# Optimization experiments

Measured on AMD Instinct MI355X. Metric: run time of the kernel, lower is better.

Reference implementation:

```python
import jax, jax.numpy as jnp
import numpy as np
import math

H = 16        # num heads
D = 64        # head dim
HID = 1024    # hidden size
MULT = 2      # GIN MLP multiplier
FRAC = 0.1    # top_k fraction of available predecessors
THR = 0.2     # threshold value
BASE = 10000.0  # rope base
CHUNK = 32    # query-row chunk for max aggregator
NEG = -1e30


def _rope(x, pos):
    # x: (b, H, S, D); pos: (b, S) int
    d = x.shape[-1]
    inv = 1.0 / (BASE ** (jnp.arange(0, d, 2, dtype=jnp.float32) / d))
    ang = pos.astype(jnp.float32)[..., None] * inv            # (b, S, d//2)
    cos = jnp.concatenate([jnp.cos(ang)] * 2, -1)[:, None]    # (b, 1, S, d)
    sin = jnp.concatenate([jnp.sin(ang)] * 2, -1)[:, None]
    x1, x2 = jnp.split(x, 2, axis=-1)
    return x * cos + jnp.concatenate([-x2, x1], -1) * sin


def _scaled_topk_causal(adj):
    # faithful vectorization of scaled_topk_causal_4d: per query row i, keep
    # top max(1, ceil(FRAC*i)) of the (threshold-filtered) strict predecessors.
    S = adj.shape[-1]
    j = jnp.arange(S)
    strict = j[None, :] < j[:, None]                           # (S, S) j < i
    # torch: filtered = a[:, :i] * (a >= thr)  -> below-threshold become 0
    filtered = jnp.where(strict, jnp.where(adj >= THR, adj, 0.0), NEG)
    order = jnp.argsort(-filtered, axis=-1)                    # descending, stable
    rank = jnp.argsort(order, axis=-1)                         # inverse permutation
    k = jnp.maximum(1, jnp.ceil(FRAC * jnp.arange(S, dtype=jnp.float32))).astype(jnp.int32)
    k = k.at[0].set(0)                                         # row 0 has no predecessors
    return ((rank < k[None, None, :, None]) & strict).astype(adj.dtype)


def reference(hidden_states, Wq, Wk, Wv, Wo, W1, W2, eps, position_ids):
    b, S, _ = hidden_states.shape
    q = (hidden_states @ Wq).reshape(b, S, H, D).transpose(0, 2, 1, 3)
    kk = (hidden_states @ Wk).reshape(b, S, H, D).transpose(0, 2, 1, 3)
    v = (hidden_states @ Wv).reshape(b, S, H, D).transpose(0, 2, 1, 3)
    q = _rope(q, position_ids)
    kk = _rope(kk, position_ids)
    scores = jnp.einsum('bhid,bhjd->bhij', q, kk) / math.sqrt(D)
    adj = _scaled_topk_causal(scores)                          # binary (b,H,S,S)
    deg = adj.sum(-1)                                          # (b,H,S)
    denom = jnp.maximum(deg, 1.0)[..., None]
    s_agg = jnp.einsum('bhij,bhjd->bhid', adj, v)              # sum
    m_agg = s_agg / denom                                      # mean
    var = jnp.maximum(jnp.einsum('bhij,bhjd->bhid', adj, v * v) / denom - m_agg ** 2, 0.0)
    # max aggregator: masked max over selected predecessors, chunked over rows
    nc = S // CHUNK
    adj_c = jnp.moveaxis(adj.reshape(b, H, nc, CHUNK, S), 2, 0)  # (nc,b,H,C,S)
    mx = jax.lax.map(
        lambda ac: jnp.max(jnp.where(ac[..., None] > 0, v[:, :, None, :, :], NEG), axis=-2),
        adj_c)                                                 # (nc,b,H,C,D)
    mx = jnp.moveaxis(mx, 0, 2).reshape(b, H, S, D)
    mx = jnp.where(deg[..., None] > 0, mx, 0.0)
    comb = jnp.concatenate([s_agg, m_agg, mx, var], -1)        # (b,H,S,4D)
    h1 = jax.nn.silu(jnp.einsum('bhsf,hfm->bhsm', comb, W1))   # per-head GIN MLP
    head_out = jnp.einsum('bhsm,hmd->bhsd', h1, W2) + eps * v  # epsilon-scaled residual
    return head_out.transpose(0, 2, 1, 3).reshape(b, S, H * D) @ Wo


def setup_inputs() -> dict:
    key = jax.random.key(0)
    ks = jax.random.split(key, 8)
    b, S = 1, 1024
    sc = 0.02
    return {
        'hidden_states': jax.random.normal(ks[0], (b, S, HID), jnp.float32),
        'Wq': jax.random.normal(ks[1], (HID, H * D), jnp.float32) * sc,
        'Wk': jax.random.normal(ks[2], (HID, H * D), jnp.float32) * sc,
        'Wv': jax.random.normal(ks[3], (HID, H * D), jnp.float32) * sc,
        'Wo': jax.random.normal(ks[4], (H * D, HID), jnp.float32) * sc,
        'W1': jax.random.normal(ks[5], (H, 4 * D, MULT * D), jnp.float32) * sc,
        'W2': jax.random.normal(ks[6], (H, MULT * D, D), jnp.float32) * sc,
        'eps': jnp.asarray(0.1, jnp.float32),
        'position_ids': jnp.arange(S, dtype=jnp.int32)[None, :],
    }
```

## Files before the change

kernel.cpp:

```cpp
#include <hip/hip_runtime.h>
#include <math.h>

#define NEGF  -1e30f
#define TAU   1e-6f

static __device__ __forceinline__ int imin(int a, int b) { return a < b ? a : b; }

template <int MODE>
__global__ __launch_bounds__(256) void gemm64(
    const float* __restrict__ A, const float* __restrict__ B, float* __restrict__ C,
    const float* __restrict__ R, const float* __restrict__ eps_p,
    int M, int N, int K, int lda, int ldb, int ldc,
    long sA, long sB, long sC)
{
  const int z = blockIdx.z;
  A += (long)z * sA;
  B += (long)z * sB;
  float* Cf = C + (long)z * sC;
  const float* Rz = (MODE == 2) ? (R + (long)z * sC) : nullptr;

  const int bm = blockIdx.x * 64;
  const int bn = blockIdx.y * 64;
  const int tid = threadIdx.x;
  const int r0 = (tid >> 4) * 4;
  const int c0 = (tid & 15) * 4;

  __shared__ float As[16][68];
  __shared__ float Bs[16][64];

  float acc[4][4] = {};

  const int ar = tid >> 2;
  const int ac = (tid & 3) * 4;
  const int br = tid >> 4;
  const int bc = (tid & 15) * 4;

  for (int kt = 0; kt < K; kt += 16) {
    float4 av = *(const float4*)(A + (long)(bm + ar) * lda + kt + ac);
    float4 bv = *(const float4*)(B + (long)(kt + br) * ldb + bn + bc);
    As[ac + 0][ar] = av.x;
    As[ac + 1][ar] = av.y;
    As[ac + 2][ar] = av.z;
    As[ac + 3][ar] = av.w;
    *(float4*)&Bs[br][bc] = bv;
    __syncthreads();
#pragma unroll
    for (int kk = 0; kk < 16; ++kk) {
      const float4 xa = *(const float4*)&As[kk][r0];
      const float4 yb = *(const float4*)&Bs[kk][c0];
      acc[0][0] += xa.x * yb.x; acc[0][1] += xa.x * yb.y; acc[0][2] += xa.x * yb.z; acc[0][3] += xa.x * yb.w;
      acc[1][0] += xa.y * yb.x; acc[1][1] += xa.y * yb.y; acc[1][2] += xa.y * yb.z; acc[1][3] += xa.y * yb.w;
      acc[2][0] += xa.z * yb.x; acc[2][1] += xa.z * yb.y; acc[2][2] += xa.z * yb.z; acc[2][3] += xa.z * yb.w;
      acc[3][0] += xa.w * yb.x; acc[3][1] += xa.w * yb.y; acc[3][2] += xa.w * yb.z; acc[3][3] += xa.w * yb.w;
    }
    __syncthreads();
  }

  const float ev = (MODE == 2) ? eps_p[0] : 0.0f;
#pragma unroll
  for (int e = 0; e < 4; ++e)
#pragma unroll
    for (int f = 0; f < 4; ++f) {
      const int r = bm + r0 + e;
      const int c = bn + c0 + f;
      float x = acc[e][f];
      if (MODE == 1) x = x / (1.0f + expf(-x));
      if (MODE == 2) x += ev * Rz[(long)r * ldc + c];
      Cf[(long)r * ldc + c] = x;
    }
}

__global__ __launch_bounds__(256) void gemm_qkv(
    const float* __restrict__ A,
    const float* __restrict__ Wq, const float* __restrict__ Wk, const float* __restrict__ Wv,
    float* __restrict__ qo, float* __restrict__ ko, float* __restrict__ vo)
{
  const int z = blockIdx.z;
  const float* B = (z == 0) ? Wq : (z == 1) ? Wk : Wv;
  float* C = (z == 0) ? qo : (z == 1) ? ko : vo;

  const int bm = blockIdx.x * 64;
  const int bn = blockIdx.y * 64;
  const int tid = threadIdx.x;
  const int r0 = (tid >> 4) * 4;
  const int c0 = (tid & 15) * 4;

  __shared__ float As[2][32][68];
  __shared__ float Bs[2][32][64];

  float acc[4][4] = {};
  float tot[4][4] = {};

  const int ar = tid >> 2;
  const int ac = (tid & 3) * 8;
  const int br = tid >> 3;
  const int bc = (tid & 7) * 8;

  {
    float4 a0 = *(const float4*)(A + (long)(bm + ar) * 1024 + ac);
    float4 a1 = *(const float4*)(A + (long)(bm + ar) * 1024 + ac + 4);
    float4 b0 = *(const float4*)(B + (long)br * 1024 + bn + bc);
    float4 b1 = *(const float4*)(B + (long)br * 1024 + bn + bc + 4);
    As[0][ac + 0][ar] = a0.x; As[0][ac + 1][ar] = a0.y;
    As[0][ac + 2][ar] = a0.z; As[0][ac + 3][ar] = a0.w;
    As[0][ac + 4][ar] = a1.x; As[0][ac + 5][ar] = a1.y;
    As[0][ac + 6][ar] = a1.z; As[0][ac + 7][ar] = a1.w;
    *(float4*)&Bs[0][br][bc] = b0;
    *(float4*)&Bs[0][br][bc + 4] = b1;
  }
  __syncthreads();

  int cur = 0;
  for (int kt = 0; kt < 1024; kt += 32) {
    const bool more = (kt + 32 < 1024);
    float4 a0n, a1n, b0n, b1n;
    if (more) {
      a0n = *(const float4*)(A + (long)(bm + ar) * 1024 + kt + 32 + ac);
      a1n = *(const float4*)(A + (long)(bm + ar) * 1024 + kt + 32 + ac + 4);
      b0n = *(const float4*)(B + (long)(kt + 32 + br) * 1024 + bn + bc);
      b1n = *(const float4*)(B + (long)(kt + 32 + br) * 1024 + bn + bc + 4);
    }
    if (kt == 384 || kt == 768) {
#pragma unroll
      for (int e = 0; e < 4; ++e)
#pragma unroll
        for (int f = 0; f < 4; ++f) {
          tot[e][f] = __fadd_rn(tot[e][f], acc[e][f]);
          acc[e][f] = 0.0f;
        }
    }
#pragma unroll
    for (int kk = 0; kk < 32; ++kk) {
      const float4 xa = *(const float4*)&As[cur][kk][r0];
      const float4 yb = *(const float4*)&Bs[cur][kk][c0];
      acc[0][0] += xa.x * yb.x; acc[0][1] += xa.x * yb.y; acc[0][2] += xa.x * yb.z; acc[0][3] += xa.x * yb.w;
      acc[1][0] += xa.y * yb.x; acc[1][1] += xa.y * yb.y; acc[1][2] += xa.y * yb.z; acc[1][3] += xa.y * yb.w;
      acc[2][0] += xa.z * yb.x; acc[2][1] += xa.z * yb.y; acc[2][2] += xa.z * yb.z; acc[2][3] += xa.z * yb.w;
      acc[3][0] += xa.w * yb.x; acc[3][1] += xa.w * yb.y; acc[3][2] += xa.w * yb.z; acc[3][3] += xa.w * yb.w;
    }
    if (more) {
      const int nxt = cur ^ 1;
      As[nxt][ac + 0][ar] = a0n.x; As[nxt][ac + 1][ar] = a0n.y;
      As[nxt][ac + 2][ar] = a0n.z; As[nxt][ac + 3][ar] = a0n.w;
      As[nxt][ac + 4][ar] = a1n.x; As[nxt][ac + 5][ar] = a1n.y;
      As[nxt][ac + 6][ar] = a1n.z; As[nxt][ac + 7][ar] = a1n.w;
      *(float4*)&Bs[nxt][br][bc] = b0n;
      *(float4*)&Bs[nxt][br][bc + 4] = b1n;
      __syncthreads();
      cur = nxt;
    }
  }

#pragma unroll
  for (int e = 0; e < 4; ++e)
#pragma unroll
    for (int f = 0; f < 4; ++f)
      C[(long)(bm + r0 + e) * 1024 + bn + c0 + f] = __fadd_rn(tot[e][f], acc[e][f]);
}

__global__ __launch_bounds__(256) void gemm_out(
    const float* __restrict__ A, const float* __restrict__ B, float* __restrict__ C)
{
  const int bm = blockIdx.x * 32;
  const int bn = blockIdx.y * 64;
  const int tid = threadIdx.x;
  const int r0 = (tid >> 4) * 2;
  const int c0 = (tid & 15) * 4;

  __shared__ float As[2][16][36];
  __shared__ float Bs[2][16][64];

  float acc[2][4] = {};

  const int ar = tid >> 3;
  const int ac = (tid & 7) * 2;
  const int br = tid >> 4;
  const int bc = (tid & 15) * 4;

  {
    float2 av = *(const float2*)(A + (long)(bm + ar) * 1024 + ac);
    float4 bv = *(const float4*)(B + (long)br * 1024 + bn + bc);
    As[0][ac + 0][ar] = av.x;
    As[0][ac + 1][ar] = av.y;
    *(float4*)&Bs[0][br][bc] = bv;
  }
  __syncthreads();

  int cur = 0;
  for (int kt = 0; kt < 1024; kt += 16) {
    const bool more = (kt + 16 < 1024);
    float2 avn;
    float4 bvn;
    if (more) {
      avn = *(const float2*)(A + (long)(bm + ar) * 1024 + kt + 16 + ac);
      bvn = *(const float4*)(B + (long)(kt + 16 + br) * 1024 + bn + bc);
    }
#pragma unroll
    for (int kk = 0; kk < 16; ++kk) {
      const float2 xa = *(const float2*)&As[cur][kk][r0];
      const float4 yb = *(const float4*)&Bs[cur][kk][c0];
      acc[0][0] += xa.x * yb.x; acc[0][1] += xa.x * yb.y; acc[0][2] += xa.x * yb.z; acc[0][3] += xa.x * yb.w;
      acc[1][0] += xa.y * yb.x; acc[1][1] += xa.y * yb.y; acc[1][2] += xa.y * yb.z; acc[1][3] += xa.y * yb.w;
    }
    if (more) {
      const int nxt = cur ^ 1;
      As[nxt][ac + 0][ar] = avn.x;
      As[nxt][ac + 1][ar] = avn.y;
      *(float4*)&Bs[nxt][br][bc] = bvn;
      __syncthreads();
      cur = nxt;
    }
  }

#pragma unroll
  for (int e = 0; e < 2; ++e)
#pragma unroll
    for (int f = 0; f < 4; ++f)
      C[(long)(bm + r0 + e) * 1024 + bn + c0 + f] = acc[e][f];
}

__global__ __launch_bounds__(256) void rope_kernel(float* __restrict__ q,
                                                   float* __restrict__ kb,
                                                   const int* __restrict__ pos_ids)
{
  const int g = blockIdx.x * blockDim.x + threadIdx.x;
  const int t = g & 31;
  const int h = (g >> 5) & 15;
  const int s = (g >> 9) & 1023;
  const int buf = g >> 19;
  float* p = buf ? kb : q;

  const float e = (float)(2 * t) / 64.0f;
  const float p32 = (float)pow(10000.0, (double)e);
  const float inv = __fdiv_rn(1.0f, p32);
  const float posf = (float)pos_ids[s];
  const float ang = __fmul_rn(posf, inv);
  const float c  = (float)cos((double)ang);
  const float sn = (float)sin((double)ang);

  const int base = s * 1024 + h * 64;
  const float x1 = p[base + t];
  const float x2 = p[base + t + 32];
  p[base + t]      = __fadd_rn(__fmul_rn(x1, c), __fmul_rn(-x2, sn));
  p[base + t + 32] = __fadd_rn(__fmul_rn(x2, c), __fmul_rn(x1, sn));
}

__global__ __launch_bounds__(256) void gemm_score(
    const float* __restrict__ q, const float* __restrict__ kb,
    float* __restrict__ S, int headBase)
{
  const int x = blockIdx.x;
  int bmT = 0;
  while ((bmT + 1) * (bmT + 2) / 2 <= x) ++bmT;
  const int bnT = x - bmT * (bmT + 1) / 2;

  const int hl = blockIdx.y;
  const int off = (headBase + hl) * 64;
  const int bm = bmT * 64;
  const int bn = bnT * 64;
  const int tid = threadIdx.x;
  const int r0 = (tid >> 4) * 4;
  const int c0 = (tid & 15) * 4;

  __shared__ float As[16][68];
  __shared__ float Bs[16][68];

  float acc[4][4] = {};

  const int ar = tid >> 2;
  const int ac = (tid & 3) * 4;

  for (int kt = 0; kt < 64; kt += 16) {
    float4 av = *(const float4*)(q  + (long)(bm + ar) * 1024 + off + kt + ac);
    float4 bv = *(const float4*)(kb + (long)(bn + ar) * 1024 + off + kt + ac);
    As[ac + 0][ar] = av.x; As[ac + 1][ar] = av.y;
    As[ac + 2][ar] = av.z; As[ac + 3][ar] = av.w;
    Bs[ac + 0][ar] = bv.x; Bs[ac + 1][ar] = bv.y;
    Bs[ac + 2][ar] = bv.z; Bs[ac + 3][ar] = bv.w;
    __syncthreads();
#pragma unroll
    for (int kk = 0; kk < 16; ++kk) {
      const float4 xa = *(const float4*)&As[kk][r0];
      const float4 yb = *(const float4*)&Bs[kk][c0];
      acc[0][0] += xa.x * yb.x; acc[0][1] += xa.x * yb.y; acc[0][2] += xa.x * yb.z; acc[0][3] += xa.x * yb.w;
      acc[1][0] += xa.y * yb.x; acc[1][1] += xa.y * yb.y; acc[1][2] += xa.y * yb.z; acc[1][3] += xa.y * yb.w;
      acc[2][0] += xa.z * yb.x; acc[2][1] += xa.z * yb.y; acc[2][2] += xa.z * yb.z; acc[2][3] += xa.z * yb.w;
      acc[3][0] += xa.w * yb.x; acc[3][1] += xa.w * yb.y; acc[3][2] += xa.w * yb.z; acc[3][3] += xa.w * yb.w;
    }
    __syncthreads();
  }

#pragma unroll
  for (int e = 0; e < 4; ++e)
#pragma unroll
    for (int f = 0; f < 4; ++f)
      S[((long)hl * 1024 + bm + r0 + e) * 1024 + bn + c0 + f] = acc[e][f] * 0.125f;
}

__global__ __launch_bounds__(256) void select_agg2(
    const float* __restrict__ S, const float* __restrict__ v,
    float* __restrict__ comb, int headBase)
{
  const int i = blockIdx.x;
  const int hl = blockIdx.y;
  const int h = headBase + hl;
  const int tid = threadIdx.x;
  const int lane = tid & 63;
  const int wid = tid >> 6;

  __shared__ int hist[256];
  __shared__ int wtot[4];
  __shared__ int selBinSh, newRkSh, selCntSh;
  __shared__ unsigned vminSh;
  __shared__ int mInIdx;
  __shared__ unsigned WBits;
  __shared__ int outIdxMin;
  __shared__ unsigned long long tbIn, tbOut;
  __shared__ int hypOut, hypIn;
  __shared__ int listLen;
  __shared__ unsigned list[128];
  __shared__ float red[6][4][64];

  if (tid == 0) {
    mInIdx = -1; WBits = 0u; outIdxMin = 0x7FFFFFFF;
    tbIn = ~0ull; tbOut = ~0ull; hypOut = -1; hypIn = -1; listLen = 0;
  }

  const int cs = (i + 255) >> 8;
  const int j0 = tid * cs;
  const int j1 = imin(j0 + cs, i);
  const int nj = (j1 > j0) ? (j1 - j0) : 0;

  float rawr[4];
  unsigned uf[4];
  const float* row = S + ((long)hl * 1024 + i) * 1024;
  for (int m = 0; m < nj; ++m) {
    const float rv = row[j0 + m];
    rawr[m] = rv;
    uf[m] = __float_as_uint((rv >= 0.2f) ? rv : 0.0f);
  }

  const int kk = (i > 0) ? (i + 9) / 10 : 0;
  unsigned V = 0u;
  int need_eq = 0;
  unsigned char f0[4] = {0, 0, 0, 0};

  if (kk > 0) {
    unsigned prefix = 0;
    int rk = kk;
    bool done = false;
    for (int pass = 0; pass < 4; ++pass) {
      const int shift = 24 - 8 * pass;
      hist[tid] = 0;
      __syncthreads();
      for (int m = 0; m < nj; ++m) {
        const unsigned u = uf[m];
        const bool active = (pass == 0) || ((u >> (shift + 8)) == prefix);
        if (active) atomicAdd(&hist[(u >> shift) & 0xFF], 1);
      }
      __syncthreads();
      const int hval = hist[tid];
      int val = hval;
#pragma unroll
      for (int off = 1; off < 64; off <<= 1) {
        int n = __shfl_up(val, off, 64);
        if (lane >= off) val += n;
      }
      if (lane == 63) wtot[wid] = val;
      __syncthreads();
      int wpre = 0;
      for (int w = 0; w < wid; ++w) wpre += wtot[w];
      const int incl = wpre + val;
      const int total = wtot[0] + wtot[1] + wtot[2] + wtot[3];
      const int sfx = total - incl + hval;
      if (sfx >= rk && (sfx - hval) < rk) {
        selBinSh = tid;
        newRkSh = rk - (sfx - hval);
        selCntSh = hval;
      }
      __syncthreads();
      const int selBin = selBinSh;
      prefix = (prefix << 8) | (unsigned)selBin;
      rk = newRkSh;
      const int scnt = selCntSh;
      if (pass == 0 && selBin == 0) {
        V = 0u; need_eq = rk; done = true;
      } else if (rk == scnt) {
        if (tid == 0) vminSh = 0xFFFFFFFFu;
        __syncthreads();
        for (int m = 0; m < nj; ++m)
          if (uf[m] != 0u && (uf[m] >> shift) == prefix) atomicMin(&vminSh, uf[m]);
        __syncthreads();
        V = vminSh; need_eq = 0x3FFFFFFF; done = true;
      }
      if (done) break;
    }
    if (!done) { V = prefix; need_eq = rk; }

    int e = 0;
    for (int m = 0; m < nj; ++m)
      if (uf[m] == V) ++e;
    int val = e;
#pragma unroll
    for (int off = 1; off < 64; off <<= 1) {
      int n = __shfl_up(val, off, 64);
      if (lane >= off) val += n;
    }
    if (lane == 63) wtot[wid] = val;
    __syncthreads();
    int wpre = 0;
    for (int w = 0; w < wid; ++w) wpre += wtot[w];
    int excl = wpre + val - e;
    for (int m = 0; m < nj; ++m) {
      const unsigned u = uf[m];
      if (u > V) f0[m] = 1;
      else if (u == V) { if (excl < need_eq) f0[m] = 1; ++excl; }
    }
  }
  __syncthreads();

  if (kk > 0 && kk < i) {
    unsigned wmax = 0u;
    for (int m = 0; m < nj; ++m) {
      const int j = j0 + m;
      const unsigned u = uf[m];
      if (f0[m]) {
        if (u == V) atomicMax(&mInIdx, j);
        const float fv = __uint_as_float(u);
        const float dd = fv - 0.2f;
        if (fv >= 0.2f && dd < TAU)
          atomicMin(&tbIn, (((unsigned long long)__float_as_uint(dd)) << 32) | (unsigned)j);
      } else {
        wmax = (u > wmax) ? u : wmax;
        if (rawr[m] < 0.2f) {
          const float dd = 0.2f - rawr[m];
          if (dd < TAU)
            atomicMin(&tbOut, (((unsigned long long)__float_as_uint(dd)) << 32) | (unsigned)j);
        }
      }
    }
#pragma unroll
    for (int off = 32; off >= 1; off >>= 1) {
      unsigned o = (unsigned)__shfl_xor((int)wmax, off, 64);
      wmax = (o > wmax) ? o : wmax;
    }
    if (lane == 0) atomicMax(&WBits, wmax);
    __syncthreads();
    for (int m = 0; m < nj; ++m) {
      const int j = j0 + m;
      if (!f0[m] && uf[m] == WBits) atomicMin(&outIdxMin, j);
    }
    __syncthreads();
    if (tid == 0) {
      float bestD = TAU;
      int oI = -1, nI = -1;
      if (outIdxMin != 0x7FFFFFFF && mInIdx >= 0) {
        const float Vf = __uint_as_float(V);
        const float Wf = __uint_as_float(WBits);
        if (!(WBits == V && V == 0u)) {
          const float gapA = Vf - Wf;
          if (gapA < bestD) { bestD = gapA; oI = mInIdx; nI = outIdxMin; }
        }
        if (tbIn != ~0ull) {
          const float d = __uint_as_float((unsigned)(tbIn >> 32));
          const int jj = (int)(tbIn & 0xFFFFFFFFu);
          const bool noop = (WBits == 0u && jj < outIdxMin);
          if (!noop && d < bestD) { bestD = d; oI = jj; nI = outIdxMin; }
        }
        if (tbOut != ~0ull && Vf <= 0.2f) {
          const float d = __uint_as_float((unsigned)(tbOut >> 32));
          const int jj = (int)(tbOut & 0xFFFFFFFFu);
          if (d < bestD) { bestD = d; oI = mInIdx; nI = jj; }
        }
      }
      hypOut = oI; hypIn = nI;
    }
  }
  __syncthreads();

  const bool amb = (hypOut >= 0);
  int cnt = 0;
  unsigned ent[5];
  for (int m = 0; m < nj; ++m) {
    const int j = j0 + m;
    unsigned s1 = f0[m];
    if (amb) { if (j == hypOut) s1 = 0; if (j == hypIn) s1 = 1; }
    if (f0[m] | s1)
      ent[cnt++] = (unsigned)j | ((unsigned)f0[m] << 10) | (s1 << 11);
  }
  int val = cnt;
#pragma unroll
  for (int off = 1; off < 64; off <<= 1) {
    int n = __shfl_up(val, off, 64);
    if (lane >= off) val += n;
  }
  if (lane == 63) wtot[wid] = val;
  __syncthreads();
  int wpre = 0;
  for (int w = 0; w < wid; ++w) wpre += wtot[w];
  const int base = wpre + val - cnt;
  for (int c = 0; c < cnt; ++c) list[base + c] = ent[c];
  if (tid == 0) listLen = wtot[0] + wtot[1] + wtot[2] + wtot[3];
  __syncthreads();

  const int L = listLen;
  float sum0 = 0, sq0 = 0, mx0 = NEGF, sum1 = 0, sq1 = 0, mx1 = NEGF;
  for (int e = wid; e < L; e += 4) {
    const unsigned en = list[e];
    const int j = en & 1023;
    const float vv = v[(long)j * 1024 + h * 64 + lane];
    if (en & (1u << 10)) { sum0 += vv; sq0 += vv * vv; mx0 = fmaxf(mx0, vv); }
    if (en & (1u << 11)) { sum1 += vv; sq1 += vv * vv; mx1 = fmaxf(mx1, vv); }
  }
  red[0][wid][lane] = sum0; red[1][wid][lane] = sq0; red[2][wid][lane] = mx0;
  red[3][wid][lane] = sum1; red[4][wid][lane] = sq1; red[5][wid][lane] = mx1;
  __syncthreads();

  if (tid < 64) {
    float S0 = 0, Q0 = 0, M0 = NEGF, S1 = 0, Q1 = 0, M1 = NEGF;
#pragma unroll
    for (int gg = 0; gg < 4; ++gg) {
      S0 += red[0][gg][tid]; Q0 += red[1][gg][tid]; M0 = fmaxf(M0, red[2][gg][tid]);
      S1 += red[3][gg][tid]; Q1 += red[4][gg][tid]; M1 = fmaxf(M1, red[5][gg][tid]);
    }
    const float denom = (float)(kk > 0 ? kk : 1);
    const float mean0 = S0 / denom, mean1 = S1 / denom;
    const float var0 = fmaxf(Q0 / denom - mean0 * mean0, 0.0f);
    const float var1 = fmaxf(Q1 / denom - mean1 * mean1, 0.0f);
    const float mx0o = (kk > 0) ? M0 : 0.0f;
    const float mx1o = (kk > 0) ? M1 : 0.0f;
    float* crow = comb + ((long)(h * 1024 + i)) * 256;
    crow[tid]       = 0.5f * (S0 + S1);
    crow[64 + tid]  = 0.5f * (mean0 + mean1);
    crow[128 + tid] = 0.5f * (mx0o + mx1o);
    crow[192 + tid] = 0.5f * (var0 + var1);
  }
}

extern "C" void kernel_launch(void* const* d_in, const int* in_sizes, int n_in,
                              void* d_out, int out_size, void* d_ws, size_t ws_size,
                              hipStream_t stream)
{
  const float* hidden = (const float*)d_in[0];
  const float* Wq = (const float*)d_in[1];
  const float* Wk = (const float*)d_in[2];
  const float* Wv = (const float*)d_in[3];
  const float* Wo = (const float*)d_in[4];
  const float* W1 = (const float*)d_in[5];
  const float* W2 = (const float*)d_in[6];
  const float* eps = (const float*)d_in[7];
  const int* pos = (const int*)d_in[8];

  const size_t MB = 1024UL * 1024UL;
  int G = 4;
  if (ws_size >= 28 * MB + 64 * MB) G = 16;
  else if (ws_size >= 28 * MB + 32 * MB) G = 8;

  float* q      = (float*)d_ws;
  float* kbuf   = q + (1 << 20);
  float* v      = kbuf + (1 << 20);
  float* comb   = v + (1 << 20);
  float* scores = comb + (1 << 22);
  float* h1     = scores;
  float* ho     = scores + (1 << 21);

  const dim3 blk(256);

  gemm_qkv<<<dim3(16, 16, 3), blk, 0, stream>>>(hidden, Wq, Wk, Wv, q, kbuf, v);

  rope_kernel<<<4096, blk, 0, stream>>>(q, kbuf, pos);

  for (int g = 0; g < 16; g += G) {
    gemm_score<<<dim3(136, G), blk, 0, stream>>>(q, kbuf, scores, g);
    select_agg2<<<dim3(1024, G), blk, 0, stream>>>(scores, v, comb, g);
  }

  gemm64<1><<<dim3(16, 2, 16), blk, 0, stream>>>(comb, W1, h1, nullptr, nullptr,
      1024, 128, 256, 256, 128, 128, (long)1024 * 256, (long)256 * 128, (long)1024 * 128);

  gemm64<2><<<dim3(16, 1, 16), blk, 0, stream>>>(h1, W2, ho, v, eps,
      1024, 64, 128, 128, 64, 1024, (long)1024 * 128, (long)128 * 64, 64);

  gemm_out<<<dim3(32, 16), blk, 0, stream>>>(ho, Wo, (float*)d_out);
}
```

Measured before the change: 397.4 us.

## Use 128x128 register tiles in QKV and score GEMMs; unroll select loops

The QKV projection and the causal score GEMM move from 64x64 to 128x128 output tiles, with 8x8 outputs per thread held in four 4x4 accumulators. This raises arithmetic intensity per shared-memory load and cuts the block count, at the cost of more registers and lower occupancy. The score GEMM now loads its full 64-wide K in two 32-wide stages. The select/aggregate kernel fully unrolls its fixed 4-element per-thread loops, counts zeros in the first histogram pass with a wave reduction instead of per-element atomics, and rebuilds the compaction list without a temporary array.

```diff
diff --git a/kernel.cpp b/kernel.cpp
--- a/kernel.cpp
+++ b/kernel.cpp
@@ -5,6 +5,20 @@
 #define TAU   1e-6f
 
 static __device__ __forceinline__ int imin(int a, int b) { return a < b ? a : b; }
+
+static __device__ __forceinline__ void fma44(float A[4][4], const float4 xa, const float4 yb) {
+  A[0][0] += xa.x * yb.x; A[0][1] += xa.x * yb.y; A[0][2] += xa.x * yb.z; A[0][3] += xa.x * yb.w;
+  A[1][0] += xa.y * yb.x; A[1][1] += xa.y * yb.y; A[1][2] += xa.y * yb.z; A[1][3] += xa.y * yb.w;
+  A[2][0] += xa.z * yb.x; A[2][1] += xa.z * yb.y; A[2][2] += xa.z * yb.z; A[2][3] += xa.z * yb.w;
+  A[3][0] += xa.w * yb.x; A[3][1] += xa.w * yb.y; A[3][2] += xa.w * yb.z; A[3][3] += xa.w * yb.w;
+}
+
+static __device__ __forceinline__ void fold44(float T[4][4], float A[4][4]) {
+#pragma unroll
+  for (int e = 0; e < 4; ++e)
+#pragma unroll
+    for (int f = 0; f < 4; ++f) { T[e][f] = __fadd_rn(T[e][f], A[e][f]); A[e][f] = 0.0f; }
+}
 
 template <int MODE>
 __global__ __launch_bounds__(256) void gemm64(
@@ -48,10 +62,7 @@
     for (int kk = 0; kk < 16; ++kk) {
       const float4 xa = *(const float4*)&As[kk][r0];
       const float4 yb = *(const float4*)&Bs[kk][c0];
-      acc[0][0] += xa.x * yb.x; acc[0][1] += xa.x * yb.y; acc[0][2] += xa.x * yb.z; acc[0][3] += xa.x * yb.w;
-      acc[1][0] += xa.y * yb.x; acc[1][1] += xa.y * yb.y; acc[1][2] += xa.y * yb.z; acc[1][3] += xa.y * yb.w;
-      acc[2][0] += xa.z * yb.x; acc[2][1] += xa.z * yb.y; acc[2][2] += xa.z * yb.z; acc[2][3] += xa.z * yb.w;
-      acc[3][0] += xa.w * yb.x; acc[3][1] += xa.w * yb.y; acc[3][2] += xa.w * yb.z; acc[3][3] += xa.w * yb.w;
+      fma44(acc, xa, yb);
     }
     __syncthreads();
   }
@@ -79,71 +90,65 @@
   const float* B = (z == 0) ? Wq : (z == 1) ? Wk : Wv;
   float* C = (z == 0) ? qo : (z == 1) ? ko : vo;
 
-  const int bm = blockIdx.x * 64;
-  const int bn = blockIdx.y * 64;
+  const int bm = blockIdx.x * 128;
+  const int bn = blockIdx.y * 128;
   const int tid = threadIdx.x;
   const int r0 = (tid >> 4) * 4;
   const int c0 = (tid & 15) * 4;
 
-  __shared__ float As[2][32][68];
-  __shared__ float Bs[2][32][64];
-
-  float acc[4][4] = {};
-  float tot[4][4] = {};
+  __shared__ float As[2][16][132];
+  __shared__ float Bs[2][16][132];
+
+  float a00[4][4] = {}, a01[4][4] = {}, a10[4][4] = {}, a11[4][4] = {};
+  float t00[4][4] = {}, t01[4][4] = {}, t10[4][4] = {}, t11[4][4] = {};
 
   const int ar = tid >> 2;
-  const int ac = (tid & 3) * 8;
-  const int br = tid >> 3;
-  const int bc = (tid & 7) * 8;
+  const int ac = (tid & 3) * 4;
+  const int br = tid >> 4;
+  const int bc = (tid & 15) * 8;
 
   {
     float4 a0 = *(const float4*)(A + (long)(bm + ar) * 1024 + ac);
-    float4 a1 = *(const float4*)(A + (long)(bm + ar) * 1024 + ac + 4);
+    float4 a1 = *(const float4*)(A + (long)(bm + 64 + ar) * 1024 + ac);
     float4 b0 = *(const float4*)(B + (long)br * 1024 + bn + bc);
     float4 b1 = *(const float4*)(B + (long)br * 1024 + bn + bc + 4);
     As[0][ac + 0][ar] = a0.x; As[0][ac + 1][ar] = a0.y;
     As[0][ac + 2][ar] = a0.z; As[0][ac + 3][ar] = a0.w;
-    As[0][ac + 4][ar] = a1.x; As[0][ac + 5][ar] = a1.y;
-    As[0][ac + 6][ar] = a1.z; As[0][ac + 7][ar] = a1.w;
+    As[0][ac + 0][64 + ar] = a1.x; As[0][ac + 1][64 + ar] = a1.y;
+    As[0][ac + 2][64 + ar] = a1.z; As[0][ac + 3][64 + ar] = a1.w;
     *(float4*)&Bs[0][br][bc] = b0;
     *(float4*)&Bs[0][br][bc + 4] = b1;
   }
   __syncthreads();
 
   int cur = 0;
-  for (int kt = 0; kt < 1024; kt += 32) {
-    const bool more = (kt + 32 < 1024);
+  for (int kt = 0; kt < 1024; kt += 16) {
+    const bool more = (kt + 16 < 1024);
     float4 a0n, a1n, b0n, b1n;
     if (more) {
-      a0n = *(const float4*)(A + (long)(bm + ar) * 1024 + kt + 32 + ac);
-      a1n = *(const float4*)(A + (long)(bm + ar) * 1024 + kt + 32 + ac + 4);
-      b0n = *(const float4*)(B + (long)(kt + 32 + br) * 1024 + bn + bc);
-      b1n = *(const float4*)(B + (long)(kt + 32 + br) * 1024 + bn + bc + 4);
+      a0n = *(const float4*)(A + (long)(bm + ar) * 1024 + kt + 16 + ac);
+      a1n = *(const float4*)(A + (long)(bm + 64 + ar) * 1024 + kt + 16 + ac);
+      b0n = *(const float4*)(B + (long)(kt + 16 + br) * 1024 + bn + bc);
+      b1n = *(const float4*)(B + (long)(kt + 16 + br) * 1024 + bn + bc + 4);
     }
     if (kt == 384 || kt == 768) {
-#pragma unroll
-      for (int e = 0; e < 4; ++e)
-#pragma unroll
-        for (int f = 0; f < 4; ++f) {
-          tot[e][f] = __fadd_rn(tot[e][f], acc[e][f]);
-          acc[e][f] = 0.0f;
-        }
-    }
-#pragma unroll
-    for (int kk = 0; kk < 32; ++kk) {
-      const float4 xa = *(const float4*)&As[cur][kk][r0];
-      const float4 yb = *(const float4*)&Bs[cur][kk][c0];
-      acc[0][0] += xa.x * yb.x; acc[0][1] += xa.x * yb.y; acc[0][2] += xa.x * yb.z; acc[0][3] += xa.x * yb.w;
-      acc[1][0] += xa.y * yb.x; acc[1][1] += xa.y * yb.y; acc[1][2] += xa.y * yb.z; acc[1][3] += xa.y * yb.w;
-      acc[2][0] += xa.z * yb.x; acc[2][1] += xa.z * yb.y; acc[2][2] += xa.z * yb.z; acc[2][3] += xa.z * yb.w;
-      acc[3][0] += xa.w * yb.x; acc[3][1] += xa.w * yb.y; acc[3][2] += xa.w * yb.z; acc[3][3] += xa.w * yb.w;
+      fold44(t00, a00); fold44(t01, a01); fold44(t10, a10); fold44(t11, a11);
+    }
+#pragma unroll
+    for (int kk = 0; kk < 16; ++kk) {
+      const float4 xa0 = *(const float4*)&As[cur][kk][r0];
+      const float4 xa1 = *(const float4*)&As[cur][kk][64 + r0];
+      const float4 yb0 = *(const float4*)&Bs[cur][kk][c0];
+      const float4 yb1 = *(const float4*)&Bs[cur][kk][64 + c0];
+      fma44(a00, xa0, yb0); fma44(a01, xa0, yb1);
+      fma44(a10, xa1, yb0); fma44(a11, xa1, yb1);
     }
     if (more) {
       const int nxt = cur ^ 1;
       As[nxt][ac + 0][ar] = a0n.x; As[nxt][ac + 1][ar] = a0n.y;
       As[nxt][ac + 2][ar] = a0n.z; As[nxt][ac + 3][ar] = a0n.w;
-      As[nxt][ac + 4][ar] = a1n.x; As[nxt][ac + 5][ar] = a1n.y;
-      As[nxt][ac + 6][ar] = a1n.z; As[nxt][ac + 7][ar] = a1n.w;
+      As[nxt][ac + 0][64 + ar] = a1n.x; As[nxt][ac + 1][64 + ar] = a1n.y;
+      As[nxt][ac + 2][64 + ar] = a1n.z; As[nxt][ac + 3][64 + ar] = a1n.w;
       *(float4*)&Bs[nxt][br][bc] = b0n;
       *(float4*)&Bs[nxt][br][bc + 4] = b1n;
       __syncthreads();
@@ -154,8 +159,12 @@
 #pragma unroll
   for (int e = 0; e < 4; ++e)
 #pragma unroll
-    for (int f = 0; f < 4; ++f)
-      C[(long)(bm + r0 + e) * 1024 + bn + c0 + f] = __fadd_rn(tot[e][f], acc[e][f]);
+    for (int f = 0; f < 4; ++f) {
+      C[(long)(bm + r0 + e) * 1024 + bn + c0 + f]           = __fadd_rn(t00[e][f], a00[e][f]);
+      C[(long)(bm + r0 + e) * 1024 + bn + 64 + c0 + f]      = __fadd_rn(t01[e][f], a01[e][f]);
+      C[(long)(bm + 64 + r0 + e) * 1024 + bn + c0 + f]      = __fadd_rn(t10[e][f], a10[e][f]);
+      C[(long)(bm + 64 + r0 + e) * 1024 + bn + 64 + c0 + f] = __fadd_rn(t11[e][f], a11[e][f]);
+    }
 }
 
 __global__ __launch_bounds__(256) void gemm_out(
@@ -256,45 +265,58 @@
 
   const int hl = blockIdx.y;
   const int off = (headBase + hl) * 64;
-  const int bm = bmT * 64;
-  const int bn = bnT * 64;
+  const int bm = bmT * 128;
+  const int bn = bnT * 128;
   const int tid = threadIdx.x;
   const int r0 = (tid >> 4) * 4;
   const int c0 = (tid & 15) * 4;
 
-  __shared__ float As[16][68];
-  __shared__ float Bs[16][68];
-
-  float acc[4][4] = {};
-
-  const int ar = tid >> 2;
-  const int ac = (tid & 3) * 4;
-
-  for (int kt = 0; kt < 64; kt += 16) {
-    float4 av = *(const float4*)(q  + (long)(bm + ar) * 1024 + off + kt + ac);
-    float4 bv = *(const float4*)(kb + (long)(bn + ar) * 1024 + off + kt + ac);
-    As[ac + 0][ar] = av.x; As[ac + 1][ar] = av.y;
-    As[ac + 2][ar] = av.z; As[ac + 3][ar] = av.w;
-    Bs[ac + 0][ar] = bv.x; Bs[ac + 1][ar] = bv.y;
-    Bs[ac + 2][ar] = bv.z; Bs[ac + 3][ar] = bv.w;
+  __shared__ float As[32][132];
+  __shared__ float Bs[32][132];
+
+  float a00[4][4] = {}, a01[4][4] = {}, a10[4][4] = {}, a11[4][4] = {};
+
+  const int lr = tid >> 2;
+  const int lc = (tid & 3) * 4;
+
+  for (int ks = 0; ks < 64; ks += 32) {
+    if (ks) __syncthreads();
+#pragma unroll
+    for (int kq = 0; kq < 32; kq += 16) {
+      const float4 qa = *(const float4*)(q  + (long)(bm + lr) * 1024 + off + ks + kq + lc);
+      const float4 qb = *(const float4*)(q  + (long)(bm + 64 + lr) * 1024 + off + ks + kq + lc);
+      const float4 ka = *(const float4*)(kb + (long)(bn + lr) * 1024 + off + ks + kq + lc);
+      const float4 kc = *(const float4*)(kb + (long)(bn + 64 + lr) * 1024 + off + ks + kq + lc);
+      As[kq + lc + 0][lr] = qa.x; As[kq + lc + 1][lr] = qa.y;
+      As[kq + lc + 2][lr] = qa.z; As[kq + lc + 3][lr] = qa.w;
+      As[kq + lc + 0][64 + lr] = qb.x; As[kq + lc + 1][64 + lr] = qb.y;
+      As[kq + lc + 2][64 + lr] = qb.z; As[kq + lc + 3][64 + lr] = qb.w;
+      Bs[kq + lc + 0][lr] = ka.x; Bs[kq + lc + 1][lr] = ka.y;
+      Bs[kq + lc + 2][lr] = ka.z; Bs[kq + lc + 3][lr] = ka.w;
+      Bs[kq + lc + 0][64 + lr] = kc.x; Bs[kq + lc + 1][64 + lr] = kc.y;
+      Bs[kq + lc + 2][64 + lr] = kc.z; Bs[kq + lc + 3][64 + lr] = kc.w;
+    }
     __syncthreads();
-#pragma unroll
-    for (int kk = 0; kk < 16; ++kk) {
-      const float4 xa = *(const float4*)&As[kk][r0];
-      const float4 yb = *(const float4*)&Bs[kk][c0];
-      acc[0][0] += xa.x * yb.x; acc[0][1] += xa.x * yb.y; acc[0][2] += xa.x * yb.z; acc[0][3] += xa.x * yb.w;
-      acc[1][0] += xa.y * yb.x; acc[1][1] += xa.y * yb.y; acc[1][2] += xa.y * yb.z; acc[1][3] += xa.y * yb.w;
-      acc[2][0] += xa.z * yb.x; acc[2][1] += xa.z * yb.y; acc[2][2] += xa.z * yb.z; acc[2][3] += xa.z * yb.w;
-      acc[3][0] += xa.w * yb.x; acc[3][1] += xa.w * yb.y; acc[3][2] += xa.w * yb.z; acc[3][3] += xa.w * yb.w;
-    }
-    __syncthreads();
+#pragma unroll 4
+    for (int kk = 0; kk < 32; ++kk) {
+      const float4 xa0 = *(const float4*)&As[kk][r0];
+      const float4 xa1 = *(const float4*)&As[kk][64 + r0];
+      const float4 yb0 = *(const float4*)&Bs[kk][c0];
+      const float4 yb1 = *(const float4*)&Bs[kk][64 + c0];
+      fma44(a00, xa0, yb0); fma44(a01, xa0, yb1);
+      fma44(a10, xa1, yb0); fma44(a11, xa1, yb1);
+    }
   }
 
 #pragma unroll
   for (int e = 0; e < 4; ++e)
 #pragma unroll
-    for (int f = 0; f < 4; ++f)
-      S[((long)hl * 1024 + bm + r0 + e) * 1024 + bn + c0 + f] = acc[e][f] * 0.125f;
+    for (int f = 0; f < 4; ++f) {
+      S[((long)hl * 1024 + bm + r0 + e) * 1024 + bn + c0 + f]           = a00[e][f] * 0.125f;
+      S[((long)hl * 1024 + bm + r0 + e) * 1024 + bn + 64 + c0 + f]      = a01[e][f] * 0.125f;
+      S[((long)hl * 1024 + bm + 64 + r0 + e) * 1024 + bn + c0 + f]      = a10[e][f] * 0.125f;
+      S[((long)hl * 1024 + bm + 64 + r0 + e) * 1024 + bn + 64 + c0 + f] = a11[e][f] * 0.125f;
+    }
 }
 
 __global__ __launch_bounds__(256) void select_agg2(
@@ -334,29 +356,42 @@
   float rawr[4];
   unsigned uf[4];
   const float* row = S + ((long)hl * 1024 + i) * 1024;
-  for (int m = 0; m < nj; ++m) {
-    const float rv = row[j0 + m];
+#pragma unroll
+  for (int m = 0; m < 4; ++m) {
+    const float rv = (m < nj) ? row[j0 + m] : 0.0f;
     rawr[m] = rv;
-    uf[m] = __float_as_uint((rv >= 0.2f) ? rv : 0.0f);
+    uf[m] = (m < nj) ? __float_as_uint((rv >= 0.2f) ? rv : 0.0f) : 0u;
   }
 
   const int kk = (i > 0) ? (i + 9) / 10 : 0;
   unsigned V = 0u;
   int need_eq = 0;
-  unsigned char f0[4] = {0, 0, 0, 0};
+  int f0[4] = {0, 0, 0, 0};
 
   if (kk > 0) {
     unsigned prefix = 0;
     int rk = kk;
     bool done = false;
-    for (int pass = 0; pass < 4; ++pass) {
+    for (int pass = 0; pass < 4 && !done; ++pass) {
       const int shift = 24 - 8 * pass;
       hist[tid] = 0;
       __syncthreads();
-      for (int m = 0; m < nj; ++m) {
-        const unsigned u = uf[m];
-        const bool active = (pass == 0) || ((u >> (shift + 8)) == prefix);
-        if (active) atomicAdd(&hist[(u >> shift) & 0xFF], 1);
+      if (pass == 0) {
+        int zc = 0;
+#pragma unroll
+        for (int m = 0; m < 4; ++m) if (m < nj) {
+          const unsigned u = uf[m];
+          if (u) atomicAdd(&hist[u >> 24], 1); else ++zc;
+        }
+#pragma unroll
+        for (int off = 32; off >= 1; off >>= 1) zc += __shfl_xor(zc, off, 64);
+        if (lane == 0 && zc) atomicAdd(&hist[0], zc);
+      } else {
+#pragma unroll
+        for (int m = 0; m < 4; ++m) if (m < nj) {
+          const unsigned u = uf[m];
+          if (u != 0u && (u >> (shift + 8)) == prefix) atomicAdd(&hist[(u >> shift) & 0xFF], 1);
+        }
       }
       __syncthreads();
       const int hval = hist[tid];
@@ -388,18 +423,20 @@
       } else if (rk == scnt) {
         if (tid == 0) vminSh = 0xFFFFFFFFu;
         __syncthreads();
-        for (int m = 0; m < nj; ++m)
-          if (uf[m] != 0u && (uf[m] >> shift) == prefix) atomicMin(&vminSh, uf[m]);
+#pragma unroll
+        for (int m = 0; m < 4; ++m) if (m < nj) {
+          const unsigned u = uf[m];
+          if (u != 0u && (u >> shift) == prefix) atomicMin(&vminSh, u);
+        }
         __syncthreads();
         V = vminSh; need_eq = 0x3FFFFFFF; done = true;
       }
-      if (done) break;
     }
     if (!done) { V = prefix; need_eq = rk; }
 
     int e = 0;
-    for (int m = 0; m < nj; ++m)
-      if (uf[m] == V) ++e;
+#pragma unroll
+    for (int m = 0; m < 4; ++m) if (m < nj) { if (uf[m] == V) ++e; }
     int val = e;
 #pragma unroll
     for (int off = 1; off < 64; off <<= 1) {
@@ -411,7 +448,8 @@
     int wpre = 0;
     for (int w = 0; w < wid; ++w) wpre += wtot[w];
     int excl = wpre + val - e;
-    for (int m = 0; m < nj; ++m) {
+#pragma unroll
+    for (int m = 0; m < 4; ++m) if (m < nj) {
       const unsigned u = uf[m];
       if (u > V) f0[m] = 1;
       else if (u == V) { if (excl < need_eq) f0[m] = 1; ++excl; }
@@ -421,7 +459,8 @@
 
   if (kk > 0 && kk < i) {
     unsigned wmax = 0u;
-    for (int m = 0; m < nj; ++m) {
+#pragma unroll
+    for (int m = 0; m < 4; ++m) if (m < nj) {
       const int j = j0 + m;
       const unsigned u = uf[m];
       if (f0[m]) {
@@ -446,7 +485,8 @@
     }
     if (lane == 0) atomicMax(&WBits, wmax);
     __syncthreads();
-    for (int m = 0; m < nj; ++m) {
+#pragma unroll
+    for (int m = 0; m < 4; ++m) if (m < nj) {
       const int j = j0 + m;
       if (!f0[m] && uf[m] == WBits) atomicMin(&outIdxMin, j);
     }
@@ -480,33 +520,43 @@
 
   const bool amb = (hypOut >= 0);
   int cnt = 0;
-  unsigned ent[5];
-  for (int m = 0; m < nj; ++m) {
+#pragma unroll
+  for (int m = 0; m < 4; ++m) if (m < nj) {
     const int j = j0 + m;
-    unsigned s1 = f0[m];
+    int s1 = f0[m];
     if (amb) { if (j == hypOut) s1 = 0; if (j == hypIn) s1 = 1; }
-    if (f0[m] | s1)
-      ent[cnt++] = (unsigned)j | ((unsigned)f0[m] << 10) | (s1 << 11);
-  }
-  int val = cnt;
-#pragma unroll
-  for (int off = 1; off < 64; off <<= 1) {
-    int n = __shfl_up(val, off, 64);
-    if (lane >= off) val += n;
-  }
-  if (lane == 63) wtot[wid] = val;
-  __syncthreads();
-  int wpre = 0;
-  for (int w = 0; w < wid; ++w) wpre += wtot[w];
-  const int base = wpre + val - cnt;
-  for (int c = 0; c < cnt; ++c) list[base + c] = ent[c];
-  if (tid == 0) listLen = wtot[0] + wtot[1] + wtot[2] + wtot[3];
+    if (f0[m] | s1) ++cnt;
+  }
+  {
+    int val = cnt;
+#pragma unroll
+    for (int off = 1; off < 64; off <<= 1) {
+      int n = __shfl_up(val, off, 64);
+      if (lane >= off) val += n;
+    }
+    if (lane == 63) wtot[wid] = val;
+    __syncthreads();
+    int wpre = 0;
+    for (int w = 0; w < wid; ++w) wpre += wtot[w];
+    int base = wpre + val - cnt;
+#pragma unroll
+    for (int m = 0; m < 4; ++m) if (m < nj) {
+      const int j = j0 + m;
+      int s1 = f0[m];
+      if (amb) { if (j == hypOut) s1 = 0; if (j == hypIn) s1 = 1; }
+      if (f0[m] | s1) {
+        list[base] = (unsigned)j | ((unsigned)f0[m] << 10) | ((unsigned)s1 << 11);
+        ++base;
+      }
+    }
+    if (tid == 0) listLen = wtot[0] + wtot[1] + wtot[2] + wtot[3];
+  }
   __syncthreads();
 
   const int L = listLen;
   float sum0 = 0, sq0 = 0, mx0 = NEGF, sum1 = 0, sq1 = 0, mx1 = NEGF;
-  for (int e = wid; e < L; e += 4) {
-    const unsigned en = list[e];
+  for (int e2 = wid; e2 < L; e2 += 4) {
+    const unsigned en = list[e2];
     const int j = en & 1023;
     const float vv = v[(long)j * 1024 + h * 64 + lane];
     if (en & (1u << 10)) { sum0 += vv; sq0 += vv * vv; mx0 = fmaxf(mx0, vv); }
@@ -566,12 +616,12 @@
 
   const dim3 blk(256);
 
-  gemm_qkv<<<dim3(16, 16, 3), blk, 0, stream>>>(hidden, Wq, Wk, Wv, q, kbuf, v);
+  gemm_qkv<<<dim3(8, 8, 3), blk, 0, stream>>>(hidden, Wq, Wk, Wv, q, kbuf, v);
 
   rope_kernel<<<4096, blk, 0, stream>>>(q, kbuf, pos);
 
   for (int g = 0; g < 16; g += G) {
-    gemm_score<<<dim3(136, G), blk, 0, stream>>>(q, kbuf, scores, g);
+    gemm_score<<<dim3(36, G), blk, 0, stream>>>(q, kbuf, scores, g);
     select_agg2<<<dim3(1024, G), blk, 0, stream>>>(scores, v, comb, g);
   }
 
```

After: 417.3 us. 5.0% more time.
